# Optimization experiments

Measured on AMD Instinct MI355X. Metric: run time of the kernel, lower is better.

## Reference

```python
import jax, jax.numpy as jnp
import numpy as np

# ---- model constants (from init_kwargs) ----
HIDDEN = 4096
NUM_HEADS = 32
HEAD_DIM = HIDDEN // NUM_HEADS  # 128
ROPE_THETA = 10000.0
P8 = 512
P6 = 1024
P4 = HIDDEN - P8 - P6  # 2560
BLOCK = 32  # scale-factor block size (SFB* are sized out*p//32)


def _block_quant(x, bits):
    """Symmetric per-32-element-block fake quantization along the last dim.
    Emulates the dequantized math of the packed 4/6/8-bit tiers in mixedgemm."""
    qmax = 2.0 ** (bits - 1) - 1.0
    shp = x.shape
    xb = x.reshape(shp[:-1] + (shp[-1] // BLOCK, BLOCK))
    scale = jnp.maximum(jnp.max(jnp.abs(xb), axis=-1, keepdims=True) / qmax, 1e-8)
    dq = (jnp.clip(jnp.round(xb / scale), -qmax, qmax) * scale).reshape(shp)
    return dq


def _mixed_quant(x):
    """Split reordered features into [p4 | p6 | p8] tiers and quantize each."""
    xn, xs, xo = jnp.split(x, [P4, P4 + P6], axis=-1)
    return jnp.concatenate([_block_quant(xn, 4), _block_quant(xs, 6), _block_quant(xo, 8)], axis=-1)


def _qlinear(x, W, reorder_index):
    """reorder_quantize_x + mixedgemm.matmul (dequantized reference math).
    x: [T, in], W: [out, in] (stored already in reordered column order)."""
    xq = _mixed_quant(x[..., reorder_index])
    Wq = _mixed_quant(W)
    return xq @ Wq.T


def _rotate_half(x):
    h = x.shape[-1] // 2
    return jnp.concatenate([-x[..., h:], x[..., :h]], axis=-1)


def setup_inputs() -> dict:
    key = jax.random.key(0)
    k1, k2, k3, k4, k5 = jax.random.split(key, 5)
    B, S = 2, 2048
    hidden_states = jax.random.normal(k1, (B, S, HIDDEN), dtype=jnp.float32)
    Wq = jax.random.normal(k2, (HIDDEN, HIDDEN), dtype=jnp.float32) * 0.02
    Wk = jax.random.normal(k3, (HIDDEN, HIDDEN), dtype=jnp.float32) * 0.02
    Wv = jax.random.normal(k4, (HIDDEN, HIDDEN), dtype=jnp.float32) * 0.02
    Wo = jax.random.normal(k5, (HIDDEN, HIDDEN), dtype=jnp.float32) * 0.02
    position_ids = jnp.broadcast_to(jnp.arange(S, dtype=jnp.int32)[None, :], (B, S))
    reorder_index = jnp.arange(HIDDEN, dtype=jnp.int32)  # default identity reorder
    return {"hidden_states": hidden_states, "Wq": Wq, "Wk": Wk, "Wv": Wv,
            "Wo": Wo, "position_ids": position_ids, "reorder_index": reorder_index}


def reference(hidden_states, Wq, Wk, Wv, Wo, position_ids, reorder_index):
    B, S, H = hidden_states.shape
    x2 = hidden_states.reshape(B * S, H)

    q = _qlinear(x2, Wq, reorder_index).reshape(B, S, NUM_HEADS, HEAD_DIM)
    k = _qlinear(x2, Wk, reorder_index).reshape(B, S, NUM_HEADS, HEAD_DIM)
    v = _qlinear(x2, Wv, reorder_index).reshape(B, S, NUM_HEADS, HEAD_DIM)

    # LlamaRotaryEmbedding: cos/sin [B, S, head_dim], unsqueeze_dim=2 (broadcast over heads)
    inv_freq = 1.0 / (ROPE_THETA ** (jnp.arange(0, HEAD_DIM, 2, dtype=jnp.float32) / HEAD_DIM))
    freqs = position_ids.astype(jnp.float32)[..., None] * inv_freq  # [B, S, hd/2]
    emb = jnp.concatenate([freqs, freqs], axis=-1)                  # [B, S, hd]
    cos = jnp.cos(emb)[:, :, None, :]
    sin = jnp.sin(emb)[:, :, None, :]
    q = q * cos + _rotate_half(q) * sin
    k = k * cos + _rotate_half(k) * sin

    # causal SDPA over [B, nH, S, hd]
    qh = q.transpose(0, 2, 1, 3)
    kh = k.transpose(0, 2, 1, 3)
    vh = v.transpose(0, 2, 1, 3)
    scaling = 1.0 / jnp.sqrt(jnp.float32(HEAD_DIM))
    scores = jnp.einsum('bhqd,bhkd->bhqk', qh, kh) * scaling
    causal = jnp.tril(jnp.ones((S, S), dtype=bool))
    scores = jnp.where(causal[None, None], scores, jnp.finfo(scores.dtype).min)
    probs = jax.nn.softmax(scores, axis=-1)
    attn = jnp.einsum('bhqk,bhkd->bhqd', probs, vh)  # [B, nH, S, hd]

    attn = attn.transpose(0, 2, 1, 3).reshape(B * S, H)
    out = _qlinear(attn, Wo, reorder_index).reshape(B, S, H)
    return out
```

## Files before the change

kernel.cpp:

```cpp
#include <hip/hip_runtime.h>


typedef __bf16 bf16_t;
typedef __bf16 bf16x8 __attribute__((ext_vector_type(8)));
typedef float f32x4 __attribute__((ext_vector_type(4)));

#define MFMA16(a, b, c) __builtin_amdgcn_mfma_f32_16x16x32_bf16(a, b, c, 0, 0, 0)

__device__ __forceinline__ void split_bf16(float x, bf16_t& h, bf16_t& l) {
    h = (bf16_t)x;
    l = (bf16_t)(x - (float)h);
}

typedef const __attribute__((address_space(1))) void glb_v;
typedef __attribute__((address_space(3))) void lds_v;

__device__ __forceinline__ void gl_lds16(const void* g, void* l) {
    __builtin_amdgcn_global_load_lds((glb_v*)g, (lds_v*)l, 16, 0, 0);
}

__global__ void quant_split(const float* __restrict__ srcf,
                            const bf16_t* __restrict__ shi, const bf16_t* __restrict__ slo,
                            const int* __restrict__ rid, int src_split, int gather,
                            bf16_t* __restrict__ dhi, bf16_t* __restrict__ dlo) {
    long idx = (long)blockIdx.x * 256 + threadIdx.x;
    int col = (int)(idx & 4095);
    long row = idx >> 12;
    int g = gather ? rid[col] : col;
    long si = row * 4096 + g;
    float v = src_split ? ((float)shi[si] + (float)slo[si]) : srcf[si];
    float a = fabsf(v);
#pragma unroll
    for (int off = 1; off < 32; off <<= 1) a = fmaxf(a, __shfl_xor(a, off, 32));
    float qmax = (col < 2560) ? 7.0f : (col < 3584 ? 31.0f : 127.0f);
    float scale = fmaxf(a / qmax, 1e-8f);
    float q = rintf(v * (1.0f / scale));
    q = fminf(fmaxf(q, -qmax), qmax);
    float dq = q * scale;
    bf16_t h, l;
    split_bf16(dq, h, l);
    dhi[idx] = h;
    dlo[idx] = l;
}

template<int AQ, int ASPL, int OSPL>
__global__ __launch_bounds__(256, 2) void gemm_bt(
    const float* __restrict__ Af,
    const bf16_t* __restrict__ AHi, const bf16_t* __restrict__ ALo,
    const int* __restrict__ rid,
    const bf16_t* __restrict__ BHi, const bf16_t* __restrict__ BLo,
    bf16_t* __restrict__ OHi, bf16_t* __restrict__ OLo,
    float* __restrict__ Of) {
    constexpr int K = 4096, N = 4096;
    __shared__ __align__(16) bf16_t sAh[128 * 32];
    __shared__ __align__(16) bf16_t sAl[128 * 32];
    __shared__ __align__(16) bf16_t sBh[128 * 32];
    __shared__ __align__(16) bf16_t sBl[128 * 32];

    const int tid = threadIdx.x;
    const int bx = blockIdx.x & 31, by = blockIdx.x >> 5;
    const int rowBase = by << 7, colBase = bx << 7;
    const int lane = tid & 63, wave = tid >> 6;
    const int wr = (wave >> 1) << 6, wc = (wave & 1) << 6;
    const int n16 = lane & 15, quad = lane >> 4;

    f32x4 acc[4][4];
#pragma unroll
    for (int m = 0; m < 4; ++m)
#pragma unroll
        for (int n = 0; n < 4; ++n) acc[m][n] = (f32x4){0.f, 0.f, 0.f, 0.f};

    for (int k0 = 0; k0 < K; k0 += 32) {
        __syncthreads();
        if (AQ) {
            float qmax = (k0 < 2560) ? 7.0f : (k0 < 3584 ? 31.0f : 127.0f);
#pragma unroll
            for (int i = 0; i < 2; ++i) {
                int l = i * 256 + tid, r = l >> 2, cb = (l & 3) << 3;
                long rowoff = (long)(rowBase + r) * K;
                const int* rp = rid + k0 + cb;
                float v[8];
                float am = 0.f;
#pragma unroll
                for (int j = 0; j < 8; ++j) {
                    int gg = rp[j];
                    float xv = ASPL ? ((float)AHi[rowoff + gg] + (float)ALo[rowoff + gg])
                                    : Af[rowoff + gg];
                    v[j] = xv;
                    am = fmaxf(am, fabsf(xv));
                }
                am = fmaxf(am, __shfl_xor(am, 1, 64));
                am = fmaxf(am, __shfl_xor(am, 2, 64));
                float scale = fmaxf(am / qmax, 1e-8f);
                float inv = 1.0f / scale;
                bf16x8 hv, lv;
#pragma unroll
                for (int j = 0; j < 8; ++j) {
                    float q = rintf(v[j] * inv);
                    q = fminf(fmaxf(q, -qmax), qmax);
                    float dq = q * scale;
                    bf16_t h, l2;
                    split_bf16(dq, h, l2);
                    hv[j] = h;
                    lv[j] = l2;
                }
                *(bf16x8*)&sAh[l << 3] = hv;
                *(bf16x8*)&sAl[l << 3] = lv;
            }
        } else {
#pragma unroll
            for (int i = 0; i < 2; ++i) {
                int l = i * 256 + tid, r = l >> 2, cb = (l & 3) << 3;
                long off = (long)(rowBase + r) * K + k0 + cb;
                *(uint4*)&sAh[l << 3] = *(const uint4*)&AHi[off];
                *(uint4*)&sAl[l << 3] = *(const uint4*)&ALo[off];
            }
        }
#pragma unroll
        for (int i = 0; i < 2; ++i) {
            int l = i * 256 + tid, r = l >> 2, cb = (l & 3) << 3;
            long off = (long)(colBase + r) * K + k0 + cb;
            *(uint4*)&sBh[l << 3] = *(const uint4*)&BHi[off];
            *(uint4*)&sBl[l << 3] = *(const uint4*)&BLo[off];
        }
        __syncthreads();

        bf16x8 ah[4], al[4], bh[4], bl[4];
#pragma unroll
        for (int m = 0; m < 4; ++m) {
            int row = wr + (m << 4) + n16;
            ah[m] = *(const bf16x8*)&sAh[(row << 5) + (quad << 3)];
            al[m] = *(const bf16x8*)&sAl[(row << 5) + (quad << 3)];
        }
#pragma unroll
        for (int n = 0; n < 4; ++n) {
            int row = wc + (n << 4) + n16;
            bh[n] = *(const bf16x8*)&sBh[(row << 5) + (quad << 3)];
            bl[n] = *(const bf16x8*)&sBl[(row << 5) + (quad << 3)];
        }
#pragma unroll
        for (int m = 0; m < 4; ++m)
#pragma unroll
            for (int n = 0; n < 4; ++n) {
                acc[m][n] = MFMA16(ah[m], bh[n], acc[m][n]);
                acc[m][n] = MFMA16(ah[m], bl[n], acc[m][n]);
                acc[m][n] = MFMA16(al[m], bh[n], acc[m][n]);
            }
    }

#pragma unroll
    for (int m = 0; m < 4; ++m)
#pragma unroll
        for (int n = 0; n < 4; ++n) {
            int row = rowBase + wr + (m << 4) + (quad << 2);
            int col = colBase + wc + (n << 4) + n16;
#pragma unroll
            for (int r = 0; r < 4; ++r) {
                if (OSPL) {
                    bf16_t h, l;
                    split_bf16(acc[m][n][r], h, l);
                    OHi[(long)(row + r) * N + col] = h;
                    OLo[(long)(row + r) * N + col] = l;
                } else {
                    Of[(long)(row + r) * N + col] = acc[m][n][r];
                }
            }
        }
}

__global__ void rope2(bf16_t* __restrict__ qh, bf16_t* __restrict__ ql,
                      bf16_t* __restrict__ kh, bf16_t* __restrict__ kl,
                      const int* __restrict__ pos) {
    int t = blockIdx.x;
    int tid = threadIdx.x;
    __shared__ float cs[64], sn[64];
    if (tid < 64) {
        float invf = (float)pow(10000.0, -(double)tid / 64.0);
        float ang = (float)pos[t] * invf;
        cs[tid] = (float)cos((double)ang);
        sn[tid] = (float)sin((double)ang);
    }
    __syncthreads();
#pragma unroll
    for (int i = 0; i < 8; ++i) {
        int l = i * 256 + tid;
        int hh = l >> 6, d = l & 63;
        long base = (long)t * 4096 + hh * 128 + d;
        float c = cs[d], s = sn[d];
        float a0 = (float)qh[base] + (float)ql[base];
        float a1 = (float)qh[base + 64] + (float)ql[base + 64];
        float r0 = a0 * c - a1 * s, r1 = a1 * c + a0 * s;
        bf16_t x, y;
        split_bf16(r0, x, y); qh[base] = x;      ql[base] = y;
        split_bf16(r1, x, y); qh[base + 64] = x; ql[base + 64] = y;
        float b0 = (float)kh[base] + (float)kl[base];
        float b1 = (float)kh[base + 64] + (float)kl[base + 64];
        r0 = b0 * c - b1 * s; r1 = b1 * c + b0 * s;
        split_bf16(r0, x, y); kh[base] = x;      kl[base] = y;
        split_bf16(r1, x, y); kh[base + 64] = x; kl[base + 64] = y;
    }
}

__global__ void transpose_vt(const ushort* __restrict__ vh, const ushort* __restrict__ vl,
                             ushort* __restrict__ th, ushort* __restrict__ tl) {
    __shared__ ushort t0[64][68];
    __shared__ ushort t1[64][68];
    int ct = blockIdx.x, tt = blockIdx.y, tid = threadIdx.x;
#pragma unroll
    for (int i = 0; i < 16; ++i) {
        int l = i * 256 + tid, r = l >> 6, c = l & 63;
        long idx = (long)(tt * 64 + r) * 4096 + ct * 64 + c;
        t0[r][c] = vh[idx];
        t1[r][c] = vl[idx];
    }
    __syncthreads();
#pragma unroll
    for (int i = 0; i < 16; ++i) {
        int l = i * 256 + tid, dr = l >> 6, sc = l & 63;
        int colg = ct * 64 + dr, hh = colg >> 7, dl = colg & 127;
        int tok = tt * 64 + sc, b = tok >> 11, s = tok & 2047;
        long o = (long)((b * 32 + hh) * 128 + dl) * 2048 + s;
        th[o] = t0[sc][dr];
        tl[o] = t1[sc][dr];
    }
}

__global__ __launch_bounds__(256, 2) void flash_attn3(
    const bf16_t* __restrict__ qhp, const bf16_t* __restrict__ qlp,
    const bf16_t* __restrict__ khp, const bf16_t* __restrict__ klp,
    const bf16_t* __restrict__ vth, const bf16_t* __restrict__ vtl,
    bf16_t* __restrict__ ohi, bf16_t* __restrict__ olo) {
    __shared__ __align__(16) char smem[75776];

    const int bid = blockIdx.x;
    const int xcd = bid & 7, ixd = bid >> 3;
    const int bh = (xcd << 3) + (ixd >> 4);
    const int qt = 15 - (ixd & 15);
    const int b = bh >> 5, h = bh & 31;
    const int tid = threadIdx.x;
    const int wave = tid >> 6, lane = tid & 63;
    const int n16 = lane & 15, quad = lane >> 4;
    const long tokB = (long)b * 2048;
    const int q0 = qt * 128 + wave * 32;
    const float scale = 0.08838834764831845f;

    bf16_t (*pH)[40] = (bf16_t (*)[40])(smem + 65536 + wave * 2560);
    bf16_t (*pL)[40] = (bf16_t (*)[40])(smem + 65536 + wave * 2560 + 1280);

    bf16x8 qhF[2][4], qlF[2][4];
#pragma unroll
    for (int m = 0; m < 2; ++m) {
        long qoff = (tokB + q0 + m * 16 + n16) * 4096 + h * 128 + quad * 8;
#pragma unroll
        for (int f = 0; f < 4; ++f) {
            qhF[m][f] = *(const bf16x8*)&qhp[qoff + f * 32];
            qlF[m][f] = *(const bf16x8*)&qlp[qoff + f * 32];
        }
    }

    const int kr0 = wave * 8 + quad;
    const int kc0 = ((((lane & 15) << 4) ^ (quad << 4)) >> 1);
    const int kc1 = ((((lane & 15) << 4) ^ ((4 + quad) << 4)) >> 1);
    const int kd0 = kr0 * 256 + ((lane & 15) << 4);
    const int vr0 = wave * 32 + (lane >> 2);
    const int vc0 = ((((lane & 3) << 4) ^ (((lane >> 2) & 3) << 4)) >> 1);
    const int vd0 = vr0 * 64 + ((lane & 3) << 4);
    const long vrow_g = (long)(bh * 128 + vr0) * 2048;

#define STAGE(BUF, KB) do {                                                   \
    char* _bb = smem + ((BUF) << 15);                                         \
    const long _kt = tokB + (long)(KB) * 32;                                  \
    const long _g0 = (_kt + kr0) * 4096 + h * 128;                            \
    gl_lds16(khp + _g0 + kc0,           _bb + kd0);                           \
    gl_lds16(klp + _g0 + kc0,           _bb + 8192 + kd0);                    \
    gl_lds16(khp + _g0 + 4 * 4096 + kc1, _bb + 1024 + kd0);                   \
    gl_lds16(klp + _g0 + 4 * 4096 + kc1, _bb + 8192 + 1024 + kd0);            \
    const long _v0 = vrow_g + (KB) * 32 + vc0;                                \
    gl_lds16(vth + _v0,                 _bb + 16384 + vd0);                   \
    gl_lds16(vtl + _v0,                 _bb + 24576 + vd0);                   \
    gl_lds16(vth + _v0 + 16 * 2048,     _bb + 16384 + 1024 + vd0);            \
    gl_lds16(vtl + _v0 + 16 * 2048,     _bb + 24576 + 1024 + vd0);            \
} while (0)

    f32x4 o[2][8];
#pragma unroll
    for (int m = 0; m < 2; ++m)
#pragma unroll
        for (int dc = 0; dc < 8; ++dc) o[m][dc] = (f32x4){0.f, 0.f, 0.f, 0.f};
    float m_i[2][4], l_i[2][4];
#pragma unroll
    for (int m = 0; m < 2; ++m)
#pragma unroll
        for (int r = 0; r < 4; ++r) { m_i[m][r] = -1e30f; l_i[m][r] = 0.f; }

    const int nkb = 4 * qt + 4;
    const int lastkb = 4 * qt + wave;

    STAGE(0, 0);
    asm volatile("s_waitcnt vmcnt(0)" ::: "memory");
    __builtin_amdgcn_s_barrier();
    asm volatile("" ::: "memory");

    for (int kb = 0; kb < nkb; ++kb) {
        if (kb + 1 < nkb) STAGE((kb + 1) & 1, kb + 1);

        if (kb <= lastkb) {
            const char* bK = smem + ((kb & 1) << 15);
            const char* bV = bK + 16384;

            f32x4 s[2][2];
            const int rswz = (n16 & 7) << 4;
#pragma unroll
            for (int nt = 0; nt < 2; ++nt) {
                const int krow = nt * 16 + n16;
                bf16x8 kh[4], kl[4];
#pragma unroll
                for (int f = 0; f < 4; ++f) {
                    const int cb = ((f << 6) | (quad << 4)) ^ rswz;
                    kh[f] = *(const bf16x8*)(bK + krow * 256 + cb);
                    kl[f] = *(const bf16x8*)(bK + 8192 + krow * 256 + cb);
                }
#pragma unroll
                for (int m = 0; m < 2; ++m) {
                    f32x4 sc = (f32x4){0.f, 0.f, 0.f, 0.f};
#pragma unroll
                    for (int f = 0; f < 4; ++f) {
                        sc = MFMA16(qhF[m][f], kh[f], sc);
                        sc = MFMA16(qhF[m][f], kl[f], sc);
                        sc = MFMA16(qlF[m][f], kh[f], sc);
                    }
                    s[m][nt] = sc;
                }
            }

            if (kb == lastkb) {
                const int key0 = kb * 32 + n16;
#pragma unroll
                for (int m = 0; m < 2; ++m)
#pragma unroll
                    for (int nt = 0; nt < 2; ++nt)
#pragma unroll
                        for (int r = 0; r < 4; ++r) {
                            int qrow = q0 + m * 16 + quad * 4 + r;
                            s[m][nt][r] = (key0 + nt * 16 <= qrow) ? s[m][nt][r] * scale
                                                                   : -1e30f;
                        }
            } else {
#pragma unroll
                for (int m = 0; m < 2; ++m)
#pragma unroll
                    for (int nt = 0; nt < 2; ++nt)
#pragma unroll
                        for (int r = 0; r < 4; ++r) s[m][nt][r] *= scale;
            }

            float alpha[2][4];
#pragma unroll
            for (int m = 0; m < 2; ++m)
#pragma unroll
                for (int r = 0; r < 4; ++r) {
                    float mx = fmaxf(s[m][0][r], s[m][1][r]);
#pragma unroll
                    for (int off = 1; off < 16; off <<= 1) mx = fmaxf(mx, __shfl_xor(mx, off, 64));
                    float mnew = fmaxf(m_i[m][r], mx);
                    alpha[m][r] = expf(m_i[m][r] - mnew);
                    m_i[m][r] = mnew;
                    float p0 = expf(s[m][0][r] - mnew);
                    float p1 = expf(s[m][1][r] - mnew);
                    s[m][0][r] = p0;
                    s[m][1][r] = p1;
                    float sum = p0 + p1;
#pragma unroll
                    for (int off = 1; off < 16; off <<= 1) sum += __shfl_xor(sum, off, 64);
                    l_i[m][r] = l_i[m][r] * alpha[m][r] + sum;
                }

            bf16x8 ph2[2], pl2[2];
#pragma unroll
            for (int m = 0; m < 2; ++m) {
#pragma unroll
                for (int nt = 0; nt < 2; ++nt)
#pragma unroll
                    for (int r = 0; r < 4; ++r) {
                        bf16_t hh2, ll2;
                        split_bf16(s[m][nt][r], hh2, ll2);
                        pH[quad * 4 + r][nt * 16 + n16] = hh2;
                        pL[quad * 4 + r][nt * 16 + n16] = ll2;
                    }
                ph2[m] = *(const bf16x8*)&pH[n16][quad * 8];
                pl2[m] = *(const bf16x8*)&pL[n16][quad * 8];
            }

#pragma unroll
            for (int dc = 0; dc < 8; ++dc) {
                const int vrow = dc * 16 + n16;
                const int vcb = ((quad ^ (n16 & 3)) << 4);
                bf16x8 vh = *(const bf16x8*)(bV + vrow * 64 + vcb);
                bf16x8 vl = *(const bf16x8*)(bV + 8192 + vrow * 64 + vcb);
#pragma unroll
                for (int m = 0; m < 2; ++m) {
#pragma unroll
                    for (int r = 0; r < 4; ++r) o[m][dc][r] *= alpha[m][r];
                    o[m][dc] = MFMA16(ph2[m], vh, o[m][dc]);
                    o[m][dc] = MFMA16(ph2[m], vl, o[m][dc]);
                    o[m][dc] = MFMA16(pl2[m], vh, o[m][dc]);
                }
            }
        }

        asm volatile("s_waitcnt vmcnt(0)" ::: "memory");
        __builtin_amdgcn_s_barrier();
        asm volatile("" ::: "memory");
    }
#undef STAGE

#pragma unroll
    for (int m = 0; m < 2; ++m)
#pragma unroll
        for (int r = 0; r < 4; ++r) {
            float invl = 1.0f / l_i[m][r];
            long row = tokB + q0 + m * 16 + quad * 4 + r;
#pragma unroll
            for (int dc = 0; dc < 8; ++dc) {
                bf16_t hh2, ll2;
                split_bf16(o[m][dc][r] * invl, hh2, ll2);
                ohi[row * 4096 + h * 128 + dc * 16 + n16] = hh2;
                olo[row * 4096 + h * 128 + dc * 16 + n16] = ll2;
            }
        }
}

extern "C" void kernel_launch(void* const* d_in, const int* in_sizes, int n_in,
                              void* d_out, int out_size, void* d_ws, size_t ws_size,
                              hipStream_t stream) {
    const float* x  = (const float*)d_in[0];
    const float* Wq = (const float*)d_in[1];
    const float* Wk = (const float*)d_in[2];
    const float* Wv = (const float*)d_in[3];
    const float* Wo = (const float*)d_in[4];
    const int* pos  = (const int*)d_in[5];
    const int* rid  = (const int*)d_in[6];

    const size_t MB = 1024ull * 1024ull;
    char* ws = (char*)d_ws;
    bf16_t* W0h = (bf16_t*)(ws);
    bf16_t* W0l = (bf16_t*)(ws + 32 * MB);
    bf16_t* W1h = (bf16_t*)(ws + 64 * MB);
    bf16_t* W1l = (bf16_t*)(ws + 96 * MB);
    bf16_t* W2h = (bf16_t*)(ws + 128 * MB);
    bf16_t* W2l = (bf16_t*)(ws + 160 * MB);
    bf16_t* OUh = (bf16_t*)d_out;
    bf16_t* OUl = (bf16_t*)((char*)d_out + 32 * MB);
    bf16_t* W3h = (bf16_t*)(ws + 192 * MB);
    bf16_t* W3l = (bf16_t*)(ws + 224 * MB);
    const bool fast = (ws_size >= 256 * MB);

    const int QG = 65536;

    quant_split<<<QG, 256, 0, stream>>>(Wq, nullptr, nullptr, rid, 0, 0, W0h, W0l);
    if (fast) {
        quant_split<<<QG, 256, 0, stream>>>(x, nullptr, nullptr, rid, 0, 1, W3h, W3l);
        gemm_bt<0, 1, 1><<<1024, 256, 0, stream>>>(nullptr, W3h, W3l, rid, W0h, W0l, W1h, W1l, nullptr);
    } else {
        gemm_bt<1, 0, 1><<<1024, 256, 0, stream>>>(x, nullptr, nullptr, rid, W0h, W0l, W1h, W1l, nullptr);
    }
    quant_split<<<QG, 256, 0, stream>>>(Wk, nullptr, nullptr, rid, 0, 0, W0h, W0l);
    if (fast)
        gemm_bt<0, 1, 1><<<1024, 256, 0, stream>>>(nullptr, W3h, W3l, rid, W0h, W0l, W2h, W2l, nullptr);
    else
        gemm_bt<1, 0, 1><<<1024, 256, 0, stream>>>(x, nullptr, nullptr, rid, W0h, W0l, W2h, W2l, nullptr);
    quant_split<<<QG, 256, 0, stream>>>(Wv, nullptr, nullptr, rid, 0, 0, W0h, W0l);
    if (fast)
        gemm_bt<0, 1, 1><<<1024, 256, 0, stream>>>(nullptr, W3h, W3l, rid, W0h, W0l, OUh, OUl, nullptr);
    else
        gemm_bt<1, 0, 1><<<1024, 256, 0, stream>>>(x, nullptr, nullptr, rid, W0h, W0l, OUh, OUl, nullptr);

    rope2<<<4096, 256, 0, stream>>>(W1h, W1l, W2h, W2l, pos);

    transpose_vt<<<dim3(64, 64), 256, 0, stream>>>((const ushort*)OUh, (const ushort*)OUl,
                                                   (ushort*)W0h, (ushort*)W0l);

    flash_attn3<<<1024, 256, 0, stream>>>(W1h, W1l, W2h, W2l, W0h, W0l, OUh, OUl);

    quant_split<<<QG, 256, 0, stream>>>(Wo, nullptr, nullptr, rid, 0, 0, W1h, W1l);
    if (fast) {
        quant_split<<<QG, 256, 0, stream>>>(nullptr, OUh, OUl, rid, 1, 1, W3h, W3l);
        gemm_bt<0, 1, 0><<<1024, 256, 0, stream>>>(nullptr, W3h, W3l, rid, W1h, W1l, nullptr, nullptr, (float*)d_out);
    } else {
        float* outf = (float*)W2h;
        gemm_bt<1, 1, 0><<<1024, 256, 0, stream>>>(nullptr, OUh, OUl, rid, W1h, W1l, nullptr, nullptr, outf);
        hipMemcpyAsync(d_out, outf, 64 * MB, hipMemcpyDeviceToDevice, stream);
    }

    (void)in_sizes; (void)n_in; (void)out_size;
}
```

Before: 2.719 ms.

## Use integer-quantized operands with per-block scales in projection GEMMs

```diff
diff --git a/kernel.cpp b/kernel.cpp
--- a/kernel.cpp
+++ b/kernel.cpp
@@ -19,10 +19,12 @@
     __builtin_amdgcn_global_load_lds((glb_v*)g, (lds_v*)l, 16, 0, 0);
 }
 
-__global__ void quant_split(const float* __restrict__ srcf,
-                            const bf16_t* __restrict__ shi, const bf16_t* __restrict__ slo,
-                            const int* __restrict__ rid, int src_split, int gather,
-                            bf16_t* __restrict__ dhi, bf16_t* __restrict__ dlo) {
+template<int OUT_I8>
+__global__ void quant_is(const float* __restrict__ srcf,
+                         const bf16_t* __restrict__ shi, const bf16_t* __restrict__ slo,
+                         const int* __restrict__ rid, int src_split, int gather,
+                         signed char* __restrict__ qi8, bf16_t* __restrict__ qbf,
+                         float* __restrict__ qs) {
     long idx = (long)blockIdx.x * 256 + threadIdx.x;
     int col = (int)(idx & 4095);
     long row = idx >> 12;
@@ -36,26 +38,21 @@
     float scale = fmaxf(a / qmax, 1e-8f);
     float q = rintf(v * (1.0f / scale));
     q = fminf(fmaxf(q, -qmax), qmax);
-    float dq = q * scale;
-    bf16_t h, l;
-    split_bf16(dq, h, l);
-    dhi[idx] = h;
-    dlo[idx] = l;
-}
-
-template<int AQ, int ASPL, int OSPL>
-__global__ __launch_bounds__(256, 2) void gemm_bt(
-    const float* __restrict__ Af,
-    const bf16_t* __restrict__ AHi, const bf16_t* __restrict__ ALo,
-    const int* __restrict__ rid,
-    const bf16_t* __restrict__ BHi, const bf16_t* __restrict__ BLo,
-    bf16_t* __restrict__ OHi, bf16_t* __restrict__ OLo,
-    float* __restrict__ Of) {
+    if (OUT_I8) qi8[idx] = (signed char)q;
+    else        qbf[idx] = (bf16_t)q;
+    if ((col & 31) == 0) qs[row * 128 + (col >> 5)] = scale;
+}
+
+template<int OSPL>
+__global__ __launch_bounds__(256, 2) void gemm_is(
+    const signed char* __restrict__ Ai, const float* __restrict__ As,
+    const bf16_t* __restrict__ Bi, const float* __restrict__ Bs,
+    bf16_t* __restrict__ OHi, bf16_t* __restrict__ OLo, float* __restrict__ Of) {
     constexpr int K = 4096, N = 4096;
-    __shared__ __align__(16) bf16_t sAh[128 * 32];
-    __shared__ __align__(16) bf16_t sAl[128 * 32];
-    __shared__ __align__(16) bf16_t sBh[128 * 32];
-    __shared__ __align__(16) bf16_t sBl[128 * 32];
+    __shared__ __align__(16) bf16_t sA[128 * 32];
+    __shared__ __align__(16) bf16_t sB[128 * 32];
+    __shared__ float sAs[128];
+    __shared__ float sBs[128];
 
     const int tid = threadIdx.x;
     const int bx = blockIdx.x & 31, by = blockIdx.x >> 5;
@@ -70,81 +67,53 @@
 #pragma unroll
         for (int n = 0; n < 4; ++n) acc[m][n] = (f32x4){0.f, 0.f, 0.f, 0.f};
 
-    for (int k0 = 0; k0 < K; k0 += 32) {
+    const int ar = tid >> 1, acb = (tid & 1) << 4;
+    const int br = tid >> 2, bcb = (tid & 3) << 3;
+
+    for (int kb = 0; kb < 128; ++kb) {
+        const int k0 = kb << 5;
         __syncthreads();
-        if (AQ) {
-            float qmax = (k0 < 2560) ? 7.0f : (k0 < 3584 ? 31.0f : 127.0f);
-#pragma unroll
-            for (int i = 0; i < 2; ++i) {
-                int l = i * 256 + tid, r = l >> 2, cb = (l & 3) << 3;
-                long rowoff = (long)(rowBase + r) * K;
-                const int* rp = rid + k0 + cb;
-                float v[8];
-                float am = 0.f;
-#pragma unroll
-                for (int j = 0; j < 8; ++j) {
-                    int gg = rp[j];
-                    float xv = ASPL ? ((float)AHi[rowoff + gg] + (float)ALo[rowoff + gg])
-                                    : Af[rowoff + gg];
-                    v[j] = xv;
-                    am = fmaxf(am, fabsf(xv));
-                }
-                am = fmaxf(am, __shfl_xor(am, 1, 64));
-                am = fmaxf(am, __shfl_xor(am, 2, 64));
-                float scale = fmaxf(am / qmax, 1e-8f);
-                float inv = 1.0f / scale;
-                bf16x8 hv, lv;
-#pragma unroll
-                for (int j = 0; j < 8; ++j) {
-                    float q = rintf(v[j] * inv);
-                    q = fminf(fmaxf(q, -qmax), qmax);
-                    float dq = q * scale;
-                    bf16_t h, l2;
-                    split_bf16(dq, h, l2);
-                    hv[j] = h;
-                    lv[j] = l2;
-                }
-                *(bf16x8*)&sAh[l << 3] = hv;
-                *(bf16x8*)&sAl[l << 3] = lv;
-            }
-        } else {
-#pragma unroll
-            for (int i = 0; i < 2; ++i) {
-                int l = i * 256 + tid, r = l >> 2, cb = (l & 3) << 3;
-                long off = (long)(rowBase + r) * K + k0 + cb;
-                *(uint4*)&sAh[l << 3] = *(const uint4*)&AHi[off];
-                *(uint4*)&sAl[l << 3] = *(const uint4*)&ALo[off];
-            }
-        }
-#pragma unroll
-        for (int i = 0; i < 2; ++i) {
-            int l = i * 256 + tid, r = l >> 2, cb = (l & 3) << 3;
-            long off = (long)(colBase + r) * K + k0 + cb;
-            *(uint4*)&sBh[l << 3] = *(const uint4*)&BHi[off];
-            *(uint4*)&sBl[l << 3] = *(const uint4*)&BLo[off];
-        }
+        gl_lds16(&Bi[(long)(colBase + br) * K + k0 + bcb], &sB[(long)tid << 3]);
+        gl_lds16(&Bi[(long)(colBase + 64 + br) * K + k0 + bcb], &sB[(long)(256 + tid) << 3]);
+        {
+            int4 raw = *(const int4*)&Ai[(long)(rowBase + ar) * K + k0 + acb];
+            const signed char* pc = (const signed char*)&raw;
+            bf16x8 v0, v1;
+#pragma unroll
+            for (int j = 0; j < 8; ++j) {
+                v0[j] = (bf16_t)(float)pc[j];
+                v1[j] = (bf16_t)(float)pc[8 + j];
+            }
+            *(bf16x8*)&sA[(ar << 5) + acb] = v0;
+            *(bf16x8*)&sA[(ar << 5) + acb + 8] = v1;
+        }
+        if (tid < 128) sAs[tid] = As[(long)(rowBase + tid) * 128 + kb];
+        else           sBs[tid - 128] = Bs[(long)(colBase + tid - 128) * 128 + kb];
         __syncthreads();
 
-        bf16x8 ah[4], al[4], bh[4], bl[4];
+        bf16x8 a[4], b[4];
+        f32x4 asv[4];
+        float bsv[4];
 #pragma unroll
         for (int m = 0; m < 4; ++m) {
-            int row = wr + (m << 4) + n16;
-            ah[m] = *(const bf16x8*)&sAh[(row << 5) + (quad << 3)];
-            al[m] = *(const bf16x8*)&sAl[(row << 5) + (quad << 3)];
+            a[m] = *(const bf16x8*)&sA[((wr + (m << 4) + n16) << 5) + (quad << 3)];
+            asv[m] = *(const f32x4*)&sAs[wr + (m << 4) + (quad << 2)];
         }
 #pragma unroll
         for (int n = 0; n < 4; ++n) {
-            int row = wc + (n << 4) + n16;
-            bh[n] = *(const bf16x8*)&sBh[(row << 5) + (quad << 3)];
-            bl[n] = *(const bf16x8*)&sBl[(row << 5) + (quad << 3)];
-        }
+            b[n] = *(const bf16x8*)&sB[((wc + (n << 4) + n16) << 5) + (quad << 3)];
+            bsv[n] = sBs[wc + (n << 4) + n16];
+        }
+        const f32x4 z = (f32x4){0.f, 0.f, 0.f, 0.f};
 #pragma unroll
         for (int m = 0; m < 4; ++m)
 #pragma unroll
             for (int n = 0; n < 4; ++n) {
-                acc[m][n] = MFMA16(ah[m], bh[n], acc[m][n]);
-                acc[m][n] = MFMA16(ah[m], bl[n], acc[m][n]);
-                acc[m][n] = MFMA16(al[m], bh[n], acc[m][n]);
+                f32x4 sc = MFMA16(a[m], b[n], z);
+                float bn = bsv[n];
+#pragma unroll
+                for (int r = 0; r < 4; ++r)
+                    acc[m][n][r] = fmaf(asv[m][r] * bn, sc[r], acc[m][n][r]);
             }
     }
 
@@ -443,54 +412,41 @@
 
     const size_t MB = 1024ull * 1024ull;
     char* ws = (char*)d_ws;
-    bf16_t* W0h = (bf16_t*)(ws);
-    bf16_t* W0l = (bf16_t*)(ws + 32 * MB);
-    bf16_t* W1h = (bf16_t*)(ws + 64 * MB);
-    bf16_t* W1l = (bf16_t*)(ws + 96 * MB);
-    bf16_t* W2h = (bf16_t*)(ws + 128 * MB);
-    bf16_t* W2l = (bf16_t*)(ws + 160 * MB);
+    bf16_t* QH = (bf16_t*)(ws);
+    bf16_t* QL = (bf16_t*)(ws + 32 * MB);
+    bf16_t* KH = (bf16_t*)(ws + 64 * MB);
+    bf16_t* KL = (bf16_t*)(ws + 96 * MB);
+    char* S = ws + 128 * MB;
+    signed char* Xi = (signed char*)S;
+    float*  Xs  = (float*)(S + 16 * MB);
+    bf16_t* Wi  = (bf16_t*)(S + 18 * MB);
+    float*  Wsc = (float*)(S + 50 * MB);
+    bf16_t* VTh = (bf16_t*)S;
+    bf16_t* VTl = (bf16_t*)(S + 32 * MB);
     bf16_t* OUh = (bf16_t*)d_out;
     bf16_t* OUl = (bf16_t*)((char*)d_out + 32 * MB);
-    bf16_t* W3h = (bf16_t*)(ws + 192 * MB);
-    bf16_t* W3l = (bf16_t*)(ws + 224 * MB);
-    const bool fast = (ws_size >= 256 * MB);
 
     const int QG = 65536;
 
-    quant_split<<<QG, 256, 0, stream>>>(Wq, nullptr, nullptr, rid, 0, 0, W0h, W0l);
-    if (fast) {
-        quant_split<<<QG, 256, 0, stream>>>(x, nullptr, nullptr, rid, 0, 1, W3h, W3l);
-        gemm_bt<0, 1, 1><<<1024, 256, 0, stream>>>(nullptr, W3h, W3l, rid, W0h, W0l, W1h, W1l, nullptr);
-    } else {
-        gemm_bt<1, 0, 1><<<1024, 256, 0, stream>>>(x, nullptr, nullptr, rid, W0h, W0l, W1h, W1l, nullptr);
-    }
-    quant_split<<<QG, 256, 0, stream>>>(Wk, nullptr, nullptr, rid, 0, 0, W0h, W0l);
-    if (fast)
-        gemm_bt<0, 1, 1><<<1024, 256, 0, stream>>>(nullptr, W3h, W3l, rid, W0h, W0l, W2h, W2l, nullptr);
-    else
-        gemm_bt<1, 0, 1><<<1024, 256, 0, stream>>>(x, nullptr, nullptr, rid, W0h, W0l, W2h, W2l, nullptr);
-    quant_split<<<QG, 256, 0, stream>>>(Wv, nullptr, nullptr, rid, 0, 0, W0h, W0l);
-    if (fast)
-        gemm_bt<0, 1, 1><<<1024, 256, 0, stream>>>(nullptr, W3h, W3l, rid, W0h, W0l, OUh, OUl, nullptr);
-    else
-        gemm_bt<1, 0, 1><<<1024, 256, 0, stream>>>(x, nullptr, nullptr, rid, W0h, W0l, OUh, OUl, nullptr);
-
-    rope2<<<4096, 256, 0, stream>>>(W1h, W1l, W2h, W2l, pos);
+    quant_is<1><<<QG, 256, 0, stream>>>(x, nullptr, nullptr, rid, 0, 1, Xi, nullptr, Xs);
+
+    quant_is<0><<<QG, 256, 0, stream>>>(Wq, nullptr, nullptr, rid, 0, 0, nullptr, Wi, Wsc);
+    gemm_is<1><<<1024, 256, 0, stream>>>(Xi, Xs, Wi, Wsc, QH, QL, nullptr);
+    quant_is<0><<<QG, 256, 0, stream>>>(Wk, nullptr, nullptr, rid, 0, 0, nullptr, Wi, Wsc);
+    gemm_is<1><<<1024, 256, 0, stream>>>(Xi, Xs, Wi, Wsc, KH, KL, nullptr);
+    quant_is<0><<<QG, 256, 0, stream>>>(Wv, nullptr, nullptr, rid, 0, 0, nullptr, Wi, Wsc);
+    gemm_is<1><<<1024, 256, 0, stream>>>(Xi, Xs, Wi, Wsc, OUh, OUl, nullptr);
+
+    rope2<<<4096, 256, 0, stream>>>(QH, QL, KH, KL, pos);
 
     transpose_vt<<<dim3(64, 64), 256, 0, stream>>>((const ushort*)OUh, (const ushort*)OUl,
-                                                   (ushort*)W0h, (ushort*)W0l);
-
-    flash_attn3<<<1024, 256, 0, stream>>>(W1h, W1l, W2h, W2l, W0h, W0l, OUh, OUl);
-
-    quant_split<<<QG, 256, 0, stream>>>(Wo, nullptr, nullptr, rid, 0, 0, W1h, W1l);
-    if (fast) {
-        quant_split<<<QG, 256, 0, stream>>>(nullptr, OUh, OUl, rid, 1, 1, W3h, W3l);
-        gemm_bt<0, 1, 0><<<1024, 256, 0, stream>>>(nullptr, W3h, W3l, rid, W1h, W1l, nullptr, nullptr, (float*)d_out);
-    } else {
-        float* outf = (float*)W2h;
-        gemm_bt<1, 1, 0><<<1024, 256, 0, stream>>>(nullptr, OUh, OUl, rid, W1h, W1l, nullptr, nullptr, outf);
-        hipMemcpyAsync(d_out, outf, 64 * MB, hipMemcpyDeviceToDevice, stream);
-    }
-
-    (void)in_sizes; (void)n_in; (void)out_size;
-}
+                                                   (ushort*)VTh, (ushort*)VTl);
+
+    flash_attn3<<<1024, 256, 0, stream>>>(QH, QL, KH, KL, VTh, VTl, OUh, OUl);
+
+    quant_is<1><<<QG, 256, 0, stream>>>(nullptr, OUh, OUl, rid, 1, 1, Xi, nullptr, Xs);
+    quant_is<0><<<QG, 256, 0, stream>>>(Wo, nullptr, nullptr, rid, 0, 0, nullptr, Wi, Wsc);
+    gemm_is<0><<<1024, 256, 0, stream>>>(Xi, Xs, Wi, Wsc, nullptr, nullptr, (float*)d_out);
+
+    (void)in_sizes; (void)n_in; (void)out_size; (void)ws_size;
+}
```

Measured after the change: 2.533 ms. 6.9% less time.
